# Kernel optimization log

Hardware: AMD Instinct MI355X
Metric: run time of the kernel (lower is better)

Reference implementation:

```python
import jax, jax.numpy as jnp
import numpy as np

N = 10000
E = 160000
NEG_SLOPE = 0.2


def gat_layer(x, src, dst, W, a_s, a_d, b, concat):
    # x: [N, F_in]; W: [H*C, F_in]; a_s, a_d: [H, C]; b: [H*C] or [C]
    n = x.shape[0]
    H, C = a_s.shape
    h = (x @ W.T).reshape(n, H, C)                      # [N, H, C]
    e_src = (h * a_s).sum(-1)                           # [N, H]
    e_dst = (h * a_d).sum(-1)                           # [N, H]
    e = jax.nn.leaky_relu(e_src[src] + e_dst[dst], NEG_SLOPE)  # [E, H]
    # segment softmax over incoming edges of each dst node
    m = jax.lax.stop_gradient(jax.ops.segment_max(e, dst, num_segments=n))
    e = jnp.exp(e - m[dst])
    denom = jax.ops.segment_sum(e, dst, num_segments=n)
    alpha = e / jnp.maximum(denom[dst], 1e-16)          # [E, H]
    out = jax.ops.segment_sum(h[src] * alpha[:, :, None], dst, num_segments=n)  # [N, H, C]
    out = out.reshape(n, H * C) if concat else out.mean(axis=1)
    return out + b


def _glorot(key, shape):
    fan = shape[-1]
    return jax.random.normal(key, shape, dtype=jnp.float32) * (1.0 / np.sqrt(fan))


def setup_inputs() -> dict:
    key = jax.random.key(0)
    ks = jax.random.split(key, 16)
    x = jax.random.normal(ks[0], (N, 50), dtype=jnp.float32)
    edge_index = jax.random.randint(ks[1], (2, E), 0, N, dtype=jnp.int64)
    return {
        "x": x,
        "edge_index": edge_index,
        "W1": _glorot(ks[2], (4 * 256, 50)),
        "as1": _glorot(ks[3], (4, 256)),
        "ad1": _glorot(ks[4], (4, 256)),
        "b1": jnp.zeros((4 * 256,), jnp.float32),
        "W2": _glorot(ks[5], (4 * 256, 1024)),
        "as2": _glorot(ks[6], (4, 256)),
        "ad2": _glorot(ks[7], (4, 256)),
        "b2": jnp.zeros((4 * 256,), jnp.float32),
        "W3": _glorot(ks[8], (6 * 121, 1024)),
        "as3": _glorot(ks[9], (6, 121)),
        "ad3": _glorot(ks[10], (6, 121)),
        "b3": jnp.zeros((121,), jnp.float32),
    }


def reference(x, edge_index, W1, as1, ad1, b1, W2, as2, ad2, b2, W3, as3, ad3, b3):
    n = x.shape[0]
    loop = jnp.arange(n, dtype=edge_index.dtype)
    src = jnp.concatenate([edge_index[0], loop])  # PyG GATConv adds self-loops by default
    dst = jnp.concatenate([edge_index[1], loop])
    h = gat_layer(x, src, dst, W1, as1, ad1, b1, True)
    h = jax.nn.elu(h)
    h = gat_layer(h, src, dst, W2, as2, ad2, b2, True) + h
    h = jax.nn.elu(h)
    h = gat_layer(h, src, dst, W3, as3, ad3, b3, False)
    return jax.nn.sigmoid(h)
```

## Files before the change

kernel.cpp:

```cpp
#include <hip/hip_runtime.h>
#include <math.h>

#define N_NODES 10000
#define E_EDGES 160000
#define E_TOT   170000
#define MAXDEG  128
#define MPAD    10112

typedef _Float16 f16x8 __attribute__((ext_vector_type(8)));
typedef _Float16 f16x4 __attribute__((ext_vector_type(4)));
typedef float    f32x4 __attribute__((ext_vector_type(4)));

__device__ __forceinline__ float leaky(float e) { return (e > 0.f) ? e : 0.2f * e; }

__global__ void count_kernel(const int* __restrict__ ei, int* __restrict__ deg) {
    int e = blockIdx.x * 256 + threadIdx.x;
    if (e >= E_TOT) return;
    int dst = (e < E_EDGES) ? ei[E_EDGES + e] : (e - E_EDGES);
    atomicAdd(&deg[dst], 1);
}

__global__ void scan_kernel(const int* __restrict__ deg, int* __restrict__ rowptr) {
    __shared__ int sums[1024];
    int t = threadIdx.x;
    const int CH = (N_NODES + 1023) / 1024;
    int base = t * CH;
    int s = 0;
    for (int j = 0; j < CH; j++) { int i = base + j; if (i < N_NODES) s += deg[i]; }
    sums[t] = s; __syncthreads();
    for (int off = 1; off < 1024; off <<= 1) {
        int v = (t >= off) ? sums[t - off] : 0;
        __syncthreads();
        sums[t] += v;
        __syncthreads();
    }
    int excl = (t == 0) ? 0 : sums[t - 1];
    for (int j = 0; j < CH; j++) {
        int i = base + j;
        if (i < N_NODES) { rowptr[i] = excl; excl += deg[i]; }
    }
    if (t == 1023) rowptr[N_NODES] = sums[1023];
}

__global__ void cursor_init(const int* __restrict__ rowptr, int* __restrict__ cursor) {
    int i = blockIdx.x * 256 + threadIdx.x;
    if (i < N_NODES) cursor[i] = rowptr[i];
}

__global__ void scatter_kernel(const int* __restrict__ ei, int* __restrict__ cursor,
                               int* __restrict__ perm_src) {
    int e = blockIdx.x * 256 + threadIdx.x;
    if (e >= E_TOT) return;
    int src, dst;
    if (e < E_EDGES) { src = ei[e]; dst = ei[E_EDGES + e]; }
    else { src = e - E_EDGES; dst = src; }
    int pos = atomicAdd(&cursor[dst], 1);
    perm_src[pos] = src;
}

__global__ void cvt_pad(const float* __restrict__ in, _Float16* __restrict__ out,
                        int rows, int cols, int colsPad, int totalPad) {
    int i = blockIdx.x * 256 + threadIdx.x;
    if (i >= totalPad) return;
    int r = i / colsPad, c = i - r * colsPad;
    float v = (r < rows && c < cols) ? in[(size_t)r * cols + c] : 0.f;
    out[i] = (_Float16)v;
}

__global__ void cvt_w3(const float* __restrict__ W3, _Float16* __restrict__ W3p) {
    int i = blockIdx.x * 256 + threadIdx.x;
    if (i >= 768 * 1024) return;
    int r = i >> 10, k = i & 1023;
    int hh = r >> 7, cc = r & 127;
    float v = (cc < 121) ? W3[(size_t)(hh * 121 + cc) * 1024 + k] : 0.f;
    W3p[i] = (_Float16)v;
}

__global__ void pad_a6(const float* __restrict__ a_s, const float* __restrict__ a_d,
                       float* __restrict__ asp, float* __restrict__ adp) {
    int i = blockIdx.x * 256 + threadIdx.x;
    if (i >= 768) return;
    int hh = i >> 7, cc = i & 127;
    asp[i] = (cc < 121) ? a_s[hh * 121 + cc] : 0.f;
    adp[i] = (cc < 121) ? a_d[hh * 121 + cc] : 0.f;
}

__global__ void zero_tail(_Float16* __restrict__ p, int start, int count) {
    int i = blockIdx.x * 256 + threadIdx.x;
    if (i < count) p[start + i] = (_Float16)0.f;
}

__device__ __forceinline__ void gload_lds(const _Float16* g, _Float16* l) {
    __builtin_amdgcn_global_load_lds(
        (const __attribute__((address_space(1))) void*)g,
        (__attribute__((address_space(3))) void*)l, 16, 0, 0);
}

__global__ __launch_bounds__(256) void gemm_mfma(const _Float16* __restrict__ A,
                                                 const _Float16* __restrict__ B,
                                                 _Float16* __restrict__ C,
                                                 int M, int Nn, int Kp, int ldc) {
    __shared__ _Float16 lds[16384];
    const int tid  = threadIdx.x;
    const int bm   = blockIdx.y * 128, bn = blockIdx.x * 128;
    const int w    = tid >> 6, lane = tid & 63;
    const int wr   = w >> 1,   wc   = w & 1;
    const int la   = lane & 15, g = lane >> 4;

    f32x4 acc[4][4] = {};

    const int srow = tid >> 3;
    const int skb0 = (tid & 7) * 16;

    for (int k0 = 0; k0 < Kp; k0 += 64) {
        __syncthreads();
#pragma unroll
        for (int i = 0; i < 4; i++) {
            int row = i * 32 + srow;
            int kb  = skb0 ^ ((row & 7) << 4);
            gload_lds(A + (size_t)(bm + row) * Kp + k0 + (kb >> 1),
                      lds + i * 2048 + w * 512);
        }
#pragma unroll
        for (int i = 0; i < 4; i++) {
            int row = i * 32 + srow;
            int kb  = skb0 ^ ((row & 7) << 4);
            gload_lds(B + (size_t)(bn + row) * Kp + k0 + (kb >> 1),
                      lds + 8192 + i * 2048 + w * 512);
        }
        asm volatile("s_waitcnt vmcnt(0)");
        __syncthreads();
#pragma unroll
        for (int s = 0; s < 2; s++) {
            f16x8 af[4], bf[4];
#pragma unroll
            for (int m = 0; m < 4; m++) {
                int r  = wr * 64 + m * 16 + la;
                int bc = (s * 64 + g * 16) ^ ((r & 7) << 4);
                af[m] = *(const f16x8*)(lds + r * 64 + (bc >> 1));
            }
#pragma unroll
            for (int n = 0; n < 4; n++) {
                int r  = wc * 64 + n * 16 + la;
                int bc = (s * 64 + g * 16) ^ ((r & 7) << 4);
                bf[n] = *(const f16x8*)(lds + 8192 + r * 64 + (bc >> 1));
            }
#pragma unroll
            for (int m = 0; m < 4; m++)
#pragma unroll
                for (int n = 0; n < 4; n++)
                    acc[m][n] = __builtin_amdgcn_mfma_f32_16x16x32_f16(af[m], bf[n], acc[m][n], 0, 0, 0);
        }
    }
#pragma unroll
    for (int m = 0; m < 4; m++) {
#pragma unroll
        for (int n = 0; n < 4; n++) {
            int col = bn + wc * 64 + n * 16 + la;
            if (col >= Nn) continue;
#pragma unroll
            for (int r = 0; r < 4; r++) {
                int row = bm + wr * 64 + m * 16 + g * 4 + r;
                if (row < M) C[(size_t)row * ldc + col] = (_Float16)acc[m][n][r];
            }
        }
    }
}

__global__ __launch_bounds__(256) void attn4(const _Float16* __restrict__ h,
        const float* __restrict__ a_s, const float* __restrict__ a_d,
        float* __restrict__ esrc, float* __restrict__ edst) {
    const int w = threadIdx.x >> 6, lane = threadIdx.x & 63;
    const int node = blockIdx.x * 4 + w;
    const _Float16* row = h + (size_t)node * 1024;
    float ps[4], pd[4];
#pragma unroll
    for (int j = 0; j < 4; j++) {
        int c0 = j * 256 + lane * 4;
        f16x4 v = *(const f16x4*)(row + c0);
        float4 sa = *(const float4*)(a_s + c0);
        float4 da = *(const float4*)(a_d + c0);
        ps[j] = (float)v[0] * sa.x + (float)v[1] * sa.y + (float)v[2] * sa.z + (float)v[3] * sa.w;
        pd[j] = (float)v[0] * da.x + (float)v[1] * da.y + (float)v[2] * da.z + (float)v[3] * da.w;
    }
#pragma unroll
    for (int j = 0; j < 4; j++) {
#pragma unroll
        for (int off = 32; off; off >>= 1) {
            ps[j] += __shfl_xor(ps[j], off);
            pd[j] += __shfl_xor(pd[j], off);
        }
    }
    if (lane == 0) {
        *(float4*)(esrc + (size_t)node * 4) = make_float4(ps[0], ps[1], ps[2], ps[3]);
        *(float4*)(edst + (size_t)node * 4) = make_float4(pd[0], pd[1], pd[2], pd[3]);
    }
}

__global__ __launch_bounds__(256) void attn6(const _Float16* __restrict__ h,
        const float* __restrict__ asp, const float* __restrict__ adp,
        float* __restrict__ esrc, float* __restrict__ edst) {
    const int w = threadIdx.x >> 6, lane = threadIdx.x & 63;
    const int node = blockIdx.x * 4 + w;
    const _Float16* row = h + (size_t)node * 768;
    float ps[3], pd[3];
#pragma unroll
    for (int j = 0; j < 3; j++) {
        int c0 = j * 256 + lane * 4;
        f16x4 v = *(const f16x4*)(row + c0);
        float4 sa = *(const float4*)(asp + c0);
        float4 da = *(const float4*)(adp + c0);
        ps[j] = (float)v[0] * sa.x + (float)v[1] * sa.y + (float)v[2] * sa.z + (float)v[3] * sa.w;
        pd[j] = (float)v[0] * da.x + (float)v[1] * da.y + (float)v[2] * da.z + (float)v[3] * da.w;
    }
#pragma unroll
    for (int j = 0; j < 3; j++) {
#pragma unroll
        for (int off = 16; off; off >>= 1) {
            ps[j] += __shfl_xor(ps[j], off);
            pd[j] += __shfl_xor(pd[j], off);
        }
    }
    if (lane == 0 || lane == 32) {
        int hb = lane >> 5;
        float* es = esrc + (size_t)node * 6;
        float* ed = edst + (size_t)node * 6;
#pragma unroll
        for (int j = 0; j < 3; j++) { es[2 * j + hb] = ps[j]; ed[2 * j + hb] = pd[j]; }
    }
}

template<int RES>
__global__ __launch_bounds__(256) void agg_big(const _Float16* __restrict__ h,
        const float* __restrict__ esrc, const float* __restrict__ edst,
        const int* __restrict__ rowptr, const int* __restrict__ perm_src,
        const float* __restrict__ bias, float* __restrict__ xbuf,
        _Float16* __restrict__ xh) {
    __shared__ int   srcs[MAXDEG];
    __shared__ float al[MAXDEG * 5];
    __shared__ float mh[4], sh[4];
    const int tid = threadIdx.x, lane = tid & 63, w = tid >> 6;
    const int d = blockIdx.x;
    const int r0 = rowptr[d];
    int deg = rowptr[d + 1] - r0;
    if (deg > MAXDEG) deg = MAXDEG;

    float ev[4];
    if (tid < deg) {
        int s = perm_src[r0 + tid];
        srcs[tid] = s;
        float4 es = *(const float4*)(esrc + (size_t)s * 4);
        float4 ed = *(const float4*)(edst + (size_t)d * 4);
        ev[0] = leaky(es.x + ed.x);
        ev[1] = leaky(es.y + ed.y);
        ev[2] = leaky(es.z + ed.z);
        ev[3] = leaky(es.w + ed.w);
#pragma unroll
        for (int j = 0; j < 4; j++) al[tid * 5 + j] = ev[j];
    }
    __syncthreads();
    {
        float v0 = (lane < deg)      ? al[lane * 5 + w]        : -1e30f;
        float v1 = (lane + 64 < deg) ? al[(lane + 64) * 5 + w] : -1e30f;
        float m = fmaxf(v0, v1);
#pragma unroll
        for (int off = 32; off; off >>= 1) m = fmaxf(m, __shfl_xor(m, off));
        float s = ((lane < deg) ? __expf(v0 - m) : 0.f)
                + ((lane + 64 < deg) ? __expf(v1 - m) : 0.f);
#pragma unroll
        for (int off = 32; off; off >>= 1) s += __shfl_xor(s, off);
        if (lane == 0) { mh[w] = m; sh[w] = 1.f / fmaxf(s, 1e-16f); }
    }
    __syncthreads();
    if (tid < deg) {
#pragma unroll
        for (int j = 0; j < 4; j++) al[tid * 5 + j] = __expf(ev[j] - mh[j]) * sh[j];
    }
    __syncthreads();

    const int c0 = tid * 4, hh = tid >> 6;
    f32x4 acc = {};
#pragma unroll 4
    for (int t = 0; t < deg; t++) {
        float a = al[t * 5 + hh];
        f16x4 v = *(const f16x4*)(h + (size_t)srcs[t] * 1024 + c0);
        acc[0] += a * (float)v[0]; acc[1] += a * (float)v[1];
        acc[2] += a * (float)v[2]; acc[3] += a * (float)v[3];
    }
    size_t o = (size_t)d * 1024 + c0;
    float4 bv = *(const float4*)(bias + c0);
    float4 r = RES ? *(const float4*)(xbuf + o) : make_float4(0.f, 0.f, 0.f, 0.f);
    float v0 = acc[0] + bv.x + r.x;
    float v1 = acc[1] + bv.y + r.y;
    float v2 = acc[2] + bv.z + r.z;
    float v3 = acc[3] + bv.w + r.w;
    v0 = (v0 > 0.f) ? v0 : expm1f(v0);
    v1 = (v1 > 0.f) ? v1 : expm1f(v1);
    v2 = (v2 > 0.f) ? v2 : expm1f(v2);
    v3 = (v3 > 0.f) ? v3 : expm1f(v3);
    *(float4*)(xbuf + o) = make_float4(v0, v1, v2, v3);
    f16x4 hv; hv[0] = (_Float16)v0; hv[1] = (_Float16)v1; hv[2] = (_Float16)v2; hv[3] = (_Float16)v3;
    *(f16x4*)(xh + o) = hv;
}

__global__ __launch_bounds__(256) void agg_final(const _Float16* __restrict__ h,
        const float* __restrict__ esrc, const float* __restrict__ edst,
        const int* __restrict__ rowptr, const int* __restrict__ perm_src,
        const float* __restrict__ b3, float* __restrict__ out) {
    __shared__ int   srcs[MAXDEG];
    __shared__ float al[MAXDEG * 7];
    __shared__ float mh[6], sh[6];
    __shared__ float sO[768];
    const int tid = threadIdx.x, lane = tid & 63, w = tid >> 6;
    const int d = blockIdx.x;
    const int r0 = rowptr[d];
    int deg = rowptr[d + 1] - r0;
    if (deg > MAXDEG) deg = MAXDEG;

    float ev[6];
    if (tid < deg) {
        int s = perm_src[r0 + tid];
        srcs[tid] = s;
        const float* pe = esrc + (size_t)s * 6;
        const float* pd = edst + (size_t)d * 6;
#pragma unroll
        for (int j = 0; j < 6; j++) ev[j] = leaky(pe[j] + pd[j]);
#pragma unroll
        for (int j = 0; j < 6; j++) al[tid * 7 + j] = ev[j];
    }
    __syncthreads();
    for (int hh = w; hh < 6; hh += 4) {
        float v0 = (lane < deg)      ? al[lane * 7 + hh]        : -1e30f;
        float v1 = (lane + 64 < deg) ? al[(lane + 64) * 7 + hh] : -1e30f;
        float m = fmaxf(v0, v1);
#pragma unroll
        for (int off = 32; off; off >>= 1) m = fmaxf(m, __shfl_xor(m, off));
        float s = ((lane < deg) ? __expf(v0 - m) : 0.f)
                + ((lane + 64 < deg) ? __expf(v1 - m) : 0.f);
#pragma unroll
        for (int off = 32; off; off >>= 1) s += __shfl_xor(s, off);
        if (lane == 0) { mh[hh] = m; sh[hh] = 1.f / fmaxf(s, 1e-16f); }
    }
    __syncthreads();
    if (tid < deg) {
#pragma unroll
        for (int j = 0; j < 6; j++) al[tid * 7 + j] = __expf(ev[j] - mh[j]) * sh[j];
    }
    __syncthreads();

    if (tid < 192) {
        const int c0 = tid * 4, hh = tid >> 5;
        f32x4 acc = {};
#pragma unroll 4
        for (int t = 0; t < deg; t++) {
            float a = al[t * 7 + hh];
            f16x4 v = *(const f16x4*)(h + (size_t)srcs[t] * 768 + c0);
            acc[0] += a * (float)v[0]; acc[1] += a * (float)v[1];
            acc[2] += a * (float)v[2]; acc[3] += a * (float)v[3];
        }
        *(f32x4*)(sO + c0) = acc;
    }
    __syncthreads();
    if (tid < 121) {
        float s = 0.f;
#pragma unroll
        for (int hh = 0; hh < 6; hh++) s += sO[hh * 128 + tid];
        s = s * (1.f / 6.f) + b3[tid];
        out[(size_t)d * 121 + tid] = 1.f / (1.f + __expf(-s));
    }
}

extern "C" void kernel_launch(void* const* d_in, const int* in_sizes, int n_in,
                              void* d_out, int out_size, void* d_ws, size_t ws_size,
                              hipStream_t stream) {
    const float* x   = (const float*)d_in[0];
    const int*   ei  = (const int*)d_in[1];
    const float* W1  = (const float*)d_in[2];
    const float* as1 = (const float*)d_in[3];
    const float* ad1 = (const float*)d_in[4];
    const float* b1  = (const float*)d_in[5];
    const float* W2  = (const float*)d_in[6];
    const float* as2 = (const float*)d_in[7];
    const float* ad2 = (const float*)d_in[8];
    const float* b2  = (const float*)d_in[9];
    const float* W3  = (const float*)d_in[10];
    const float* as3 = (const float*)d_in[11];
    const float* ad3 = (const float*)d_in[12];
    const float* b3  = (const float*)d_in[13];
    float* out = (float*)d_out;

    float* fws  = (float*)d_ws;
    float* xbuf = fws;
    float* esrc = fws + 10240000;
    float* edst = fws + 10300000;
    float* asp  = fws + 10360000;
    float* adp  = fws + 10360768;
    int*   iws  = (int*)(fws + 10361536);
    int* deg    = iws;
    int* rowptr = iws + N_NODES;
    int* cursor = iws + 2 * N_NODES + 1;
    int* perm   = iws + 3 * N_NODES + 1;
    _Float16* f16b = (_Float16*)(fws + 10561544);
    _Float16* xh  = f16b;
    _Float16* xh1 = xh + (size_t)MPAD * 1024;
    _Float16* W1h = xh1 + (size_t)MPAD * 64;
    _Float16* W2h = W1h + 1024 * 64;
    _Float16* W3p = W2h + 1024 * 1024;
    _Float16* h16 = W3p + 768 * 1024;

    hipMemsetAsync(deg, 0, N_NODES * sizeof(int), stream);
    count_kernel<<<(E_TOT + 255) / 256, 256, 0, stream>>>(ei, deg);
    scan_kernel<<<1, 1024, 0, stream>>>(deg, rowptr);
    cursor_init<<<(N_NODES + 255) / 256, 256, 0, stream>>>(rowptr, cursor);
    scatter_kernel<<<(E_TOT + 255) / 256, 256, 0, stream>>>(ei, cursor, perm);

    dim3 blk(256);
    cvt_pad<<<(MPAD * 64 + 255) / 256, blk, 0, stream>>>(x, xh1, N_NODES, 50, 64, MPAD * 64);
    cvt_pad<<<(1024 * 64 + 255) / 256, blk, 0, stream>>>(W1, W1h, 1024, 50, 64, 1024 * 64);
    cvt_pad<<<(1024 * 1024 + 255) / 256, blk, 0, stream>>>(W2, W2h, 1024, 1024, 1024, 1024 * 1024);
    cvt_w3<<<(768 * 1024 + 255) / 256, blk, 0, stream>>>(W3, W3p);
    pad_a6<<<3, blk, 0, stream>>>(as3, ad3, asp, adp);
    zero_tail<<<((MPAD - N_NODES) * 1024 + 255) / 256, blk, 0, stream>>>(xh, N_NODES * 1024, (MPAD - N_NODES) * 1024);

    {
        dim3 g(8, 79);
        gemm_mfma<<<g, blk, 0, stream>>>(xh1, W1h, h16, N_NODES, 1024, 64, 1024);
        attn4<<<N_NODES / 4, blk, 0, stream>>>(h16, as1, ad1, esrc, edst);
        agg_big<0><<<N_NODES, blk, 0, stream>>>(h16, esrc, edst, rowptr, perm, b1, xbuf, xh);
    }
    {
        dim3 g(8, 79);
        gemm_mfma<<<g, blk, 0, stream>>>(xh, W2h, h16, N_NODES, 1024, 1024, 1024);
        attn4<<<N_NODES / 4, blk, 0, stream>>>(h16, as2, ad2, esrc, edst);
        agg_big<1><<<N_NODES, blk, 0, stream>>>(h16, esrc, edst, rowptr, perm, b2, xbuf, xh);
    }
    {
        dim3 g(6, 79);
        gemm_mfma<<<g, blk, 0, stream>>>(xh, W3p, h16, N_NODES, 768, 1024, 768);
        attn6<<<N_NODES / 4, blk, 0, stream>>>(h16, asp, adp, esrc, edst);
        agg_final<<<N_NODES, blk, 0, stream>>>(h16, esrc, edst, rowptr, perm, b3, out);
    }
}
```

Measured before the change: 317.2 us.

## Fuse attention scores into GEMM epilogue, merge prep kernels, two nodes per aggregation block

Computes the per-head source/destination attention dot products in the GEMM epilogue with shuffle reductions and atomics, which removes the separate attn4/attn6 passes that re-read h. All weight conversion, padding and zeroing kernels become one launch, and cursor init is folded into the scan. The aggregation kernels now handle two destination nodes per block with 8-wide f16 loads. In exchange it adds memsets and float atomics, so the attention score sums depend on atomic ordering and are not bit-deterministic.

```diff
diff --git a/kernel.cpp b/kernel.cpp
--- a/kernel.cpp
+++ b/kernel.cpp
@@ -20,7 +20,8 @@
     atomicAdd(&deg[dst], 1);
 }
 
-__global__ void scan_kernel(const int* __restrict__ deg, int* __restrict__ rowptr) {
+__global__ void scan_kernel(const int* __restrict__ deg, int* __restrict__ rowptr,
+                            int* __restrict__ cursor) {
     __shared__ int sums[1024];
     int t = threadIdx.x;
     const int CH = (N_NODES + 1023) / 1024;
@@ -37,14 +38,9 @@
     int excl = (t == 0) ? 0 : sums[t - 1];
     for (int j = 0; j < CH; j++) {
         int i = base + j;
-        if (i < N_NODES) { rowptr[i] = excl; excl += deg[i]; }
+        if (i < N_NODES) { rowptr[i] = excl; cursor[i] = excl; excl += deg[i]; }
     }
     if (t == 1023) rowptr[N_NODES] = sums[1023];
-}
-
-__global__ void cursor_init(const int* __restrict__ rowptr, int* __restrict__ cursor) {
-    int i = blockIdx.x * 256 + threadIdx.x;
-    if (i < N_NODES) cursor[i] = rowptr[i];
 }
 
 __global__ void scatter_kernel(const int* __restrict__ ei, int* __restrict__ cursor,
@@ -58,36 +54,51 @@
     perm_src[pos] = src;
 }
 
-__global__ void cvt_pad(const float* __restrict__ in, _Float16* __restrict__ out,
-                        int rows, int cols, int colsPad, int totalPad) {
+#define SEG0 (MPAD * 64)
+#define SEG1 (1024 * 64)
+#define SEG2 (1024 * 1024)
+#define SEG3 (768 * 1024)
+#define SEG4 768
+#define SEG5 ((MPAD - N_NODES) * 1024)
+#define CVT_TOTAL (SEG0 + SEG1 + SEG2 + SEG3 + SEG4 + SEG5)
+
+__global__ void cvt_all(const float* __restrict__ x, const float* __restrict__ W1,
+                        const float* __restrict__ W2, const float* __restrict__ W3,
+                        const float* __restrict__ as3, const float* __restrict__ ad3,
+                        _Float16* __restrict__ xh1, _Float16* __restrict__ W1h,
+                        _Float16* __restrict__ W2h, _Float16* __restrict__ W3p,
+                        float* __restrict__ asp, float* __restrict__ adp,
+                        _Float16* __restrict__ xh) {
     int i = blockIdx.x * 256 + threadIdx.x;
-    if (i >= totalPad) return;
-    int r = i / colsPad, c = i - r * colsPad;
-    float v = (r < rows && c < cols) ? in[(size_t)r * cols + c] : 0.f;
-    out[i] = (_Float16)v;
-}
-
-__global__ void cvt_w3(const float* __restrict__ W3, _Float16* __restrict__ W3p) {
-    int i = blockIdx.x * 256 + threadIdx.x;
-    if (i >= 768 * 1024) return;
-    int r = i >> 10, k = i & 1023;
-    int hh = r >> 7, cc = r & 127;
-    float v = (cc < 121) ? W3[(size_t)(hh * 121 + cc) * 1024 + k] : 0.f;
-    W3p[i] = (_Float16)v;
-}
-
-__global__ void pad_a6(const float* __restrict__ a_s, const float* __restrict__ a_d,
-                       float* __restrict__ asp, float* __restrict__ adp) {
-    int i = blockIdx.x * 256 + threadIdx.x;
-    if (i >= 768) return;
-    int hh = i >> 7, cc = i & 127;
-    asp[i] = (cc < 121) ? a_s[hh * 121 + cc] : 0.f;
-    adp[i] = (cc < 121) ? a_d[hh * 121 + cc] : 0.f;
-}
-
-__global__ void zero_tail(_Float16* __restrict__ p, int start, int count) {
-    int i = blockIdx.x * 256 + threadIdx.x;
-    if (i < count) p[start + i] = (_Float16)0.f;
+    if (i < SEG0) {
+        int r = i >> 6, c = i & 63;
+        xh1[i] = (r < N_NODES && c < 50) ? (_Float16)x[r * 50 + c] : (_Float16)0.f;
+        return;
+    }
+    i -= SEG0;
+    if (i < SEG1) {
+        int r = i >> 6, c = i & 63;
+        W1h[i] = (c < 50) ? (_Float16)W1[r * 50 + c] : (_Float16)0.f;
+        return;
+    }
+    i -= SEG1;
+    if (i < SEG2) { W2h[i] = (_Float16)W2[i]; return; }
+    i -= SEG2;
+    if (i < SEG3) {
+        int r = i >> 10, k = i & 1023;
+        int hh = r >> 7, cc = r & 127;
+        W3p[i] = (cc < 121) ? (_Float16)W3[(size_t)(hh * 121 + cc) * 1024 + k] : (_Float16)0.f;
+        return;
+    }
+    i -= SEG3;
+    if (i < SEG4) {
+        int hh = i >> 7, cc = i & 127;
+        asp[i] = (cc < 121) ? as3[hh * 121 + cc] : 0.f;
+        adp[i] = (cc < 121) ? ad3[hh * 121 + cc] : 0.f;
+        return;
+    }
+    i -= SEG4;
+    if (i < SEG5) xh[N_NODES * 1024 + i] = (_Float16)0.f;
 }
 
 __device__ __forceinline__ void gload_lds(const _Float16* g, _Float16* l) {
@@ -96,10 +107,15 @@
         (__attribute__((address_space(3))) void*)l, 16, 0, 0);
 }
 
-__global__ __launch_bounds__(256) void gemm_mfma(const _Float16* __restrict__ A,
+template<int HSHIFT>
+__global__ __launch_bounds__(256) void gemm_attn(const _Float16* __restrict__ A,
                                                  const _Float16* __restrict__ B,
                                                  _Float16* __restrict__ C,
-                                                 int M, int Nn, int Kp, int ldc) {
+                                                 const float* __restrict__ a_s,
+                                                 const float* __restrict__ a_d,
+                                                 float* __restrict__ esrc,
+                                                 float* __restrict__ edst,
+                                                 int M, int Nn, int Kp, int ldc, int H) {
     __shared__ _Float16 lds[16384];
     const int tid  = threadIdx.x;
     const int bm   = blockIdx.y * 128, bn = blockIdx.x * 128;
@@ -165,68 +181,37 @@
             }
         }
     }
-}
-
-__global__ __launch_bounds__(256) void attn4(const _Float16* __restrict__ h,
-        const float* __restrict__ a_s, const float* __restrict__ a_d,
-        float* __restrict__ esrc, float* __restrict__ edst) {
-    const int w = threadIdx.x >> 6, lane = threadIdx.x & 63;
-    const int node = blockIdx.x * 4 + w;
-    const _Float16* row = h + (size_t)node * 1024;
-    float ps[4], pd[4];
-#pragma unroll
-    for (int j = 0; j < 4; j++) {
-        int c0 = j * 256 + lane * 4;
-        f16x4 v = *(const f16x4*)(row + c0);
-        float4 sa = *(const float4*)(a_s + c0);
-        float4 da = *(const float4*)(a_d + c0);
-        ps[j] = (float)v[0] * sa.x + (float)v[1] * sa.y + (float)v[2] * sa.z + (float)v[3] * sa.w;
-        pd[j] = (float)v[0] * da.x + (float)v[1] * da.y + (float)v[2] * da.z + (float)v[3] * da.w;
-    }
-#pragma unroll
-    for (int j = 0; j < 4; j++) {
-#pragma unroll
-        for (int off = 32; off; off >>= 1) {
-            ps[j] += __shfl_xor(ps[j], off);
-            pd[j] += __shfl_xor(pd[j], off);
-        }
-    }
-    if (lane == 0) {
-        *(float4*)(esrc + (size_t)node * 4) = make_float4(ps[0], ps[1], ps[2], ps[3]);
-        *(float4*)(edst + (size_t)node * 4) = make_float4(pd[0], pd[1], pd[2], pd[3]);
-    }
-}
-
-__global__ __launch_bounds__(256) void attn6(const _Float16* __restrict__ h,
-        const float* __restrict__ asp, const float* __restrict__ adp,
-        float* __restrict__ esrc, float* __restrict__ edst) {
-    const int w = threadIdx.x >> 6, lane = threadIdx.x & 63;
-    const int node = blockIdx.x * 4 + w;
-    const _Float16* row = h + (size_t)node * 768;
-    float ps[3], pd[3];
-#pragma unroll
-    for (int j = 0; j < 3; j++) {
-        int c0 = j * 256 + lane * 4;
-        f16x4 v = *(const f16x4*)(row + c0);
-        float4 sa = *(const float4*)(asp + c0);
-        float4 da = *(const float4*)(adp + c0);
-        ps[j] = (float)v[0] * sa.x + (float)v[1] * sa.y + (float)v[2] * sa.z + (float)v[3] * sa.w;
-        pd[j] = (float)v[0] * da.x + (float)v[1] * da.y + (float)v[2] * da.z + (float)v[3] * da.w;
-    }
-#pragma unroll
-    for (int j = 0; j < 3; j++) {
-#pragma unroll
-        for (int off = 16; off; off >>= 1) {
-            ps[j] += __shfl_xor(ps[j], off);
-            pd[j] += __shfl_xor(pd[j], off);
-        }
-    }
-    if (lane == 0 || lane == 32) {
-        int hb = lane >> 5;
-        float* es = esrc + (size_t)node * 6;
-        float* ed = edst + (size_t)node * 6;
-#pragma unroll
-        for (int j = 0; j < 3; j++) { es[2 * j + hb] = ps[j]; ed[2 * j + hb] = pd[j]; }
+    {
+        const int hh = (bn + wc * 64) >> HSHIFT;
+        float as_n[4], ad_n[4];
+#pragma unroll
+        for (int n = 0; n < 4; n++) {
+            int col = bn + wc * 64 + n * 16 + la;
+            as_n[n] = a_s[col];
+            ad_n[n] = a_d[col];
+        }
+#pragma unroll
+        for (int m = 0; m < 4; m++) {
+#pragma unroll
+            for (int r = 0; r < 4; r++) {
+                float s1 = acc[m][0][r] * as_n[0] + acc[m][1][r] * as_n[1]
+                         + acc[m][2][r] * as_n[2] + acc[m][3][r] * as_n[3];
+                float s2 = acc[m][0][r] * ad_n[0] + acc[m][1][r] * ad_n[1]
+                         + acc[m][2][r] * ad_n[2] + acc[m][3][r] * ad_n[3];
+#pragma unroll
+                for (int off = 1; off < 16; off <<= 1) {
+                    s1 += __shfl_xor(s1, off);
+                    s2 += __shfl_xor(s2, off);
+                }
+                if (la == 0) {
+                    int row = bm + wr * 64 + m * 16 + g * 4 + r;
+                    if (row < M) {
+                        atomicAdd(&esrc[(size_t)row * H + hh], s1);
+                        atomicAdd(&edst[(size_t)row * H + hh], s2);
+                    }
+                }
+            }
+        }
     }
 }
 
@@ -236,19 +221,23 @@
         const int* __restrict__ rowptr, const int* __restrict__ perm_src,
         const float* __restrict__ bias, float* __restrict__ xbuf,
         _Float16* __restrict__ xh) {
-    __shared__ int   srcs[MAXDEG];
-    __shared__ float al[MAXDEG * 5];
-    __shared__ float mh[4], sh[4];
-    const int tid = threadIdx.x, lane = tid & 63, w = tid >> 6;
-    const int d = blockIdx.x;
+    __shared__ int   srcs[2][MAXDEG];
+    __shared__ float al[2][MAXDEG * 5];
+    __shared__ float mh[2][4], sh[2][4];
+    __shared__ int   degs[2];
+    const int tid = threadIdx.x;
+    const int sub = tid >> 7, stid = tid & 127;
+    const int lane = tid & 63, w = tid >> 6, wsub = w >> 1;
+    const int d = blockIdx.x * 2 + sub;
     const int r0 = rowptr[d];
     int deg = rowptr[d + 1] - r0;
     if (deg > MAXDEG) deg = MAXDEG;
+    if (stid == 0) degs[sub] = deg;
 
     float ev[4];
-    if (tid < deg) {
-        int s = perm_src[r0 + tid];
-        srcs[tid] = s;
+    if (stid < deg) {
+        int s = perm_src[r0 + stid];
+        srcs[sub][stid] = s;
         float4 es = *(const float4*)(esrc + (size_t)s * 4);
         float4 ed = *(const float4*)(edst + (size_t)d * 4);
         ev[0] = leaky(es.x + ed.x);
@@ -256,117 +245,148 @@
         ev[2] = leaky(es.z + ed.z);
         ev[3] = leaky(es.w + ed.w);
 #pragma unroll
-        for (int j = 0; j < 4; j++) al[tid * 5 + j] = ev[j];
-    }
-    __syncthreads();
-    {
-        float v0 = (lane < deg)      ? al[lane * 5 + w]        : -1e30f;
-        float v1 = (lane + 64 < deg) ? al[(lane + 64) * 5 + w] : -1e30f;
-        float m = fmaxf(v0, v1);
-#pragma unroll
-        for (int off = 32; off; off >>= 1) m = fmaxf(m, __shfl_xor(m, off));
-        float s = ((lane < deg) ? __expf(v0 - m) : 0.f)
-                + ((lane + 64 < deg) ? __expf(v1 - m) : 0.f);
-#pragma unroll
-        for (int off = 32; off; off >>= 1) s += __shfl_xor(s, off);
-        if (lane == 0) { mh[w] = m; sh[w] = 1.f / fmaxf(s, 1e-16f); }
-    }
-    __syncthreads();
-    if (tid < deg) {
-#pragma unroll
-        for (int j = 0; j < 4; j++) al[tid * 5 + j] = __expf(ev[j] - mh[j]) * sh[j];
-    }
-    __syncthreads();
-
-    const int c0 = tid * 4, hh = tid >> 6;
-    f32x4 acc = {};
+        for (int j = 0; j < 4; j++) al[sub][stid * 5 + j] = ev[j];
+    }
+    __syncthreads();
+    {
+        int degw = degs[wsub];
+#pragma unroll
+        for (int jj = 0; jj < 2; jj++) {
+            int hh = (w & 1) * 2 + jj;
+            float v0 = (lane < degw)      ? al[wsub][lane * 5 + hh]        : -1e30f;
+            float v1 = (lane + 64 < degw) ? al[wsub][(lane + 64) * 5 + hh] : -1e30f;
+            float m = fmaxf(v0, v1);
+#pragma unroll
+            for (int off = 32; off; off >>= 1) m = fmaxf(m, __shfl_xor(m, off));
+            float s = ((lane < degw) ? __expf(v0 - m) : 0.f)
+                    + ((lane + 64 < degw) ? __expf(v1 - m) : 0.f);
+#pragma unroll
+            for (int off = 32; off; off >>= 1) s += __shfl_xor(s, off);
+            if (lane == 0) { mh[wsub][hh] = m; sh[wsub][hh] = 1.f / fmaxf(s, 1e-16f); }
+        }
+    }
+    __syncthreads();
+    if (stid < deg) {
+#pragma unroll
+        for (int j = 0; j < 4; j++) al[sub][stid * 5 + j] = __expf(ev[j] - mh[sub][j]) * sh[sub][j];
+    }
+    __syncthreads();
+
+    const int c0 = stid * 8, hh = stid >> 5;
+    float acc[8] = {};
+    const float* myal = al[sub];
+    const int* mysrc = srcs[sub];
 #pragma unroll 4
     for (int t = 0; t < deg; t++) {
-        float a = al[t * 5 + hh];
-        f16x4 v = *(const f16x4*)(h + (size_t)srcs[t] * 1024 + c0);
-        acc[0] += a * (float)v[0]; acc[1] += a * (float)v[1];
-        acc[2] += a * (float)v[2]; acc[3] += a * (float)v[3];
+        float a = myal[t * 5 + hh];
+        f16x8 v = *(const f16x8*)(h + (size_t)mysrc[t] * 1024 + c0);
+#pragma unroll
+        for (int j = 0; j < 8; j++) acc[j] += a * (float)v[j];
     }
     size_t o = (size_t)d * 1024 + c0;
-    float4 bv = *(const float4*)(bias + c0);
-    float4 r = RES ? *(const float4*)(xbuf + o) : make_float4(0.f, 0.f, 0.f, 0.f);
-    float v0 = acc[0] + bv.x + r.x;
-    float v1 = acc[1] + bv.y + r.y;
-    float v2 = acc[2] + bv.z + r.z;
-    float v3 = acc[3] + bv.w + r.w;
-    v0 = (v0 > 0.f) ? v0 : expm1f(v0);
-    v1 = (v1 > 0.f) ? v1 : expm1f(v1);
-    v2 = (v2 > 0.f) ? v2 : expm1f(v2);
-    v3 = (v3 > 0.f) ? v3 : expm1f(v3);
-    *(float4*)(xbuf + o) = make_float4(v0, v1, v2, v3);
-    f16x4 hv; hv[0] = (_Float16)v0; hv[1] = (_Float16)v1; hv[2] = (_Float16)v2; hv[3] = (_Float16)v3;
-    *(f16x4*)(xh + o) = hv;
+    f16x8 hv;
+#pragma unroll
+    for (int q = 0; q < 2; q++) {
+        float4 bv = *(const float4*)(bias + c0 + q * 4);
+        float4 r = RES ? *(const float4*)(xbuf + o + q * 4) : make_float4(0.f, 0.f, 0.f, 0.f);
+        float v0 = acc[q * 4 + 0] + bv.x + r.x;
+        float v1 = acc[q * 4 + 1] + bv.y + r.y;
+        float v2 = acc[q * 4 + 2] + bv.z + r.z;
+        float v3 = acc[q * 4 + 3] + bv.w + r.w;
+        v0 = (v0 > 0.f) ? v0 : expm1f(v0);
+        v1 = (v1 > 0.f) ? v1 : expm1f(v1);
+        v2 = (v2 > 0.f) ? v2 : expm1f(v2);
+        v3 = (v3 > 0.f) ? v3 : expm1f(v3);
+        *(float4*)(xbuf + o + q * 4) = make_float4(v0, v1, v2, v3);
+        hv[q * 4 + 0] = (_Float16)v0; hv[q * 4 + 1] = (_Float16)v1;
+        hv[q * 4 + 2] = (_Float16)v2; hv[q * 4 + 3] = (_Float16)v3;
+    }
+    *(f16x8*)(xh + o) = hv;
 }
 
 __global__ __launch_bounds__(256) void agg_final(const _Float16* __restrict__ h,
         const float* __restrict__ esrc, const float* __restrict__ edst,
         const int* __restrict__ rowptr, const int* __restrict__ perm_src,
         const float* __restrict__ b3, float* __restrict__ out) {
-    __shared__ int   srcs[MAXDEG];
-    __shared__ float al[MAXDEG * 7];
-    __shared__ float mh[6], sh[6];
-    __shared__ float sO[768];
-    const int tid = threadIdx.x, lane = tid & 63, w = tid >> 6;
-    const int d = blockIdx.x;
+    __shared__ int   srcs[2][MAXDEG];
+    __shared__ float al[2][MAXDEG * 7];
+    __shared__ float mh[2][6], sh[2][6];
+    __shared__ float sO[2][768];
+    __shared__ int   degs[2];
+    const int tid = threadIdx.x;
+    const int sub = tid >> 7, stid = tid & 127;
+    const int lane = tid & 63, w = tid >> 6, wsub = w >> 1;
+    const int d = blockIdx.x * 2 + sub;
     const int r0 = rowptr[d];
     int deg = rowptr[d + 1] - r0;
     if (deg > MAXDEG) deg = MAXDEG;
+    if (stid == 0) degs[sub] = deg;
 
     float ev[6];
-    if (tid < deg) {
-        int s = perm_src[r0 + tid];
-        srcs[tid] = s;
+    if (stid < deg) {
+        int s = perm_src[r0 + stid];
+        srcs[sub][stid] = s;
         const float* pe = esrc + (size_t)s * 6;
         const float* pd = edst + (size_t)d * 6;
-#pragma unroll
-        for (int j = 0; j < 6; j++) ev[j] = leaky(pe[j] + pd[j]);
-#pragma unroll
-        for (int j = 0; j < 6; j++) al[tid * 7 + j] = ev[j];
-    }
-    __syncthreads();
-    for (int hh = w; hh < 6; hh += 4) {
-        float v0 = (lane < deg)      ? al[lane * 7 + hh]        : -1e30f;
-        float v1 = (lane + 64 < deg) ? al[(lane + 64) * 7 + hh] : -1e30f;
-        float m = fmaxf(v0, v1);
-#pragma unroll
-        for (int off = 32; off; off >>= 1) m = fmaxf(m, __shfl_xor(m, off));
-        float s = ((lane < deg) ? __expf(v0 - m) : 0.f)
-                + ((lane + 64 < deg) ? __expf(v1 - m) : 0.f);
-#pragma unroll
-        for (int off = 32; off; off >>= 1) s += __shfl_xor(s, off);
-        if (lane == 0) { mh[hh] = m; sh[hh] = 1.f / fmaxf(s, 1e-16f); }
-    }
-    __syncthreads();
-    if (tid < deg) {
-#pragma unroll
-        for (int j = 0; j < 6; j++) al[tid * 7 + j] = __expf(ev[j] - mh[j]) * sh[j];
-    }
-    __syncthreads();
-
-    if (tid < 192) {
-        const int c0 = tid * 4, hh = tid >> 5;
-        f32x4 acc = {};
+        float2 e0 = *(const float2*)(pe);
+        float2 e1 = *(const float2*)(pe + 2);
+        float2 e2 = *(const float2*)(pe + 4);
+        float2 d0 = *(const float2*)(pd);
+        float2 d1 = *(const float2*)(pd + 2);
+        float2 d2 = *(const float2*)(pd + 4);
+        ev[0] = leaky(e0.x + d0.x); ev[1] = leaky(e0.y + d0.y);
+        ev[2] = leaky(e1.x + d1.x); ev[3] = leaky(e1.y + d1.y);
+        ev[4] = leaky(e2.x + d2.x); ev[5] = leaky(e2.y + d2.y);
+#pragma unroll
+        for (int j = 0; j < 6; j++) al[sub][stid * 7 + j] = ev[j];
+    }
+    __syncthreads();
+    {
+        int degw = degs[wsub];
+#pragma unroll
+        for (int jj = 0; jj < 3; jj++) {
+            int hh = (w & 1) * 3 + jj;
+            float v0 = (lane < degw)      ? al[wsub][lane * 7 + hh]        : -1e30f;
+            float v1 = (lane + 64 < degw) ? al[wsub][(lane + 64) * 7 + hh] : -1e30f;
+            float m = fmaxf(v0, v1);
+#pragma unroll
+            for (int off = 32; off; off >>= 1) m = fmaxf(m, __shfl_xor(m, off));
+            float s = ((lane < degw) ? __expf(v0 - m) : 0.f)
+                    + ((lane + 64 < degw) ? __expf(v1 - m) : 0.f);
+#pragma unroll
+            for (int off = 32; off; off >>= 1) s += __shfl_xor(s, off);
+            if (lane == 0) { mh[wsub][hh] = m; sh[wsub][hh] = 1.f / fmaxf(s, 1e-16f); }
+        }
+    }
+    __syncthreads();
+    if (stid < deg) {
+#pragma unroll
+        for (int j = 0; j < 6; j++) al[sub][stid * 7 + j] = __expf(ev[j] - mh[sub][j]) * sh[sub][j];
+    }
+    __syncthreads();
+
+    if (stid < 96) {
+        const int c0 = stid * 8, hh = stid >> 4;
+        float acc[8] = {};
+        const float* myal = al[sub];
+        const int* mysrc = srcs[sub];
 #pragma unroll 4
         for (int t = 0; t < deg; t++) {
-            float a = al[t * 7 + hh];
-            f16x4 v = *(const f16x4*)(h + (size_t)srcs[t] * 768 + c0);
-            acc[0] += a * (float)v[0]; acc[1] += a * (float)v[1];
-            acc[2] += a * (float)v[2]; acc[3] += a * (float)v[3];
-        }
-        *(f32x4*)(sO + c0) = acc;
-    }
-    __syncthreads();
-    if (tid < 121) {
+            float a = myal[t * 7 + hh];
+            f16x8 v = *(const f16x8*)(h + (size_t)mysrc[t] * 768 + c0);
+#pragma unroll
+            for (int j = 0; j < 8; j++) acc[j] += a * (float)v[j];
+        }
+        *(f32x4*)(sO[sub] + c0)     = *(f32x4*)(acc);
+        *(f32x4*)(sO[sub] + c0 + 4) = *(f32x4*)(acc + 4);
+    }
+    __syncthreads();
+    if (stid < 121) {
         float s = 0.f;
 #pragma unroll
-        for (int hh = 0; hh < 6; hh++) s += sO[hh * 128 + tid];
-        s = s * (1.f / 6.f) + b3[tid];
-        out[(size_t)d * 121 + tid] = 1.f / (1.f + __expf(-s));
+        for (int hh = 0; hh < 6; hh++) s += sO[sub][hh * 128 + stid];
+        s = s * (1.f / 6.f) + b3[stid];
+        out[(size_t)d * 121 + stid] = 1.f / (1.f + __expf(-s));
     }
 }
 
@@ -410,34 +430,32 @@
 
     hipMemsetAsync(deg, 0, N_NODES * sizeof(int), stream);
     count_kernel<<<(E_TOT + 255) / 256, 256, 0, stream>>>(ei, deg);
-    scan_kernel<<<1, 1024, 0, stream>>>(deg, rowptr);
-    cursor_init<<<(N_NODES + 255) / 256, 256, 0, stream>>>(rowptr, cursor);
+    scan_kernel<<<1, 1024, 0, stream>>>(deg, rowptr, cursor);
     scatter_kernel<<<(E_TOT + 255) / 256, 256, 0, stream>>>(ei, cursor, perm);
 
     dim3 blk(256);
-    cvt_pad<<<(MPAD * 64 + 255) / 256, blk, 0, stream>>>(x, xh1, N_NODES, 50, 64, MPAD * 64);
-    cvt_pad<<<(1024 * 64 + 255) / 256, blk, 0, stream>>>(W1, W1h, 1024, 50, 64, 1024 * 64);
-    cvt_pad<<<(1024 * 1024 + 255) / 256, blk, 0, stream>>>(W2, W2h, 1024, 1024, 1024, 1024 * 1024);
-    cvt_w3<<<(768 * 1024 + 255) / 256, blk, 0, stream>>>(W3, W3p);
-    pad_a6<<<3, blk, 0, stream>>>(as3, ad3, asp, adp);
-    zero_tail<<<((MPAD - N_NODES) * 1024 + 255) / 256, blk, 0, stream>>>(xh, N_NODES * 1024, (MPAD - N_NODES) * 1024);
-
-    {
+    cvt_all<<<(CVT_TOTAL + 255) / 256, blk, 0, stream>>>(x, W1, W2, W3, as3, ad3,
+                                                          xh1, W1h, W2h, W3p, asp, adp, xh);
+
+    {
+        hipMemsetAsync(esrc, 0, 120000 * sizeof(float), stream);
         dim3 g(8, 79);
-        gemm_mfma<<<g, blk, 0, stream>>>(xh1, W1h, h16, N_NODES, 1024, 64, 1024);
-        attn4<<<N_NODES / 4, blk, 0, stream>>>(h16, as1, ad1, esrc, edst);
-        agg_big<0><<<N_NODES, blk, 0, stream>>>(h16, esrc, edst, rowptr, perm, b1, xbuf, xh);
-    }
-    {
+        gemm_attn<8><<<g, blk, 0, stream>>>(xh1, W1h, h16, as1, ad1, esrc, edst,
+                                            N_NODES, 1024, 64, 1024, 4);
+        agg_big<0><<<N_NODES / 2, blk, 0, stream>>>(h16, esrc, edst, rowptr, perm, b1, xbuf, xh);
+    }
+    {
+        hipMemsetAsync(esrc, 0, 120000 * sizeof(float), stream);
         dim3 g(8, 79);
-        gemm_mfma<<<g, blk, 0, stream>>>(xh, W2h, h16, N_NODES, 1024, 1024, 1024);
-        attn4<<<N_NODES / 4, blk, 0, stream>>>(h16, as2, ad2, esrc, edst);
-        agg_big<1><<<N_NODES, blk, 0, stream>>>(h16, esrc, edst, rowptr, perm, b2, xbuf, xh);
-    }
-    {
+        gemm_attn<8><<<g, blk, 0, stream>>>(xh, W2h, h16, as2, ad2, esrc, edst,
+                                            N_NODES, 1024, 1024, 1024, 4);
+        agg_big<1><<<N_NODES / 2, blk, 0, stream>>>(h16, esrc, edst, rowptr, perm, b2, xbuf, xh);
+    }
+    {
+        hipMemsetAsync(esrc, 0, 120000 * sizeof(float), stream);
         dim3 g(6, 79);
-        gemm_mfma<<<g, blk, 0, stream>>>(xh, W3p, h16, N_NODES, 768, 1024, 768);
-        attn6<<<N_NODES / 4, blk, 0, stream>>>(h16, asp, adp, esrc, edst);
-        agg_final<<<N_NODES, blk, 0, stream>>>(h16, esrc, edst, rowptr, perm, b3, out);
-    }
-}
+        gemm_attn<7><<<g, blk, 0, stream>>>(xh, W3p, h16, asp, adp, esrc, edst,
+                                            N_NODES, 768, 1024, 768, 6);
+        agg_final<<<N_NODES / 2, blk, 0, stream>>>(h16, esrc, edst, rowptr, perm, b3, out);
+    }
+}
```

After: 343.1 us. +8.2%, slower.
